# Optimization experiments

Measured on AMD Instinct MI355X. Metric: run time of the kernel, lower is better.

The kernel has to match this reference:

```python
import jax, jax.numpy as jnp
import numpy as np

V = 1024      # visible_size (channel_size)
H = 2048      # hidden_size
F = V + H     # full_size
T = 64        # timesteps
REC = 0.8     # params['lambda']


def setup_inputs() -> dict:
    key = jax.random.key(0)
    k1, k2, k3 = jax.random.split(key, 3)
    X = jax.random.normal(k1, (T, V), jnp.float32)
    # scale W so tanh does not fully saturate (fan-in scaling, like default init)
    W = jax.random.normal(k2, (F, F), jnp.float32) / np.float32(np.sqrt(F))
    b = jax.random.normal(k3, (F,), jnp.float32) * 0.01
    # Lambda: visible block = REC, hidden block = 1, diagonal of visible block = 1
    lam = jnp.concatenate(
        [jnp.full((V, V), REC, jnp.float32), jnp.ones((V, H), jnp.float32)], axis=1
    )
    lam = lam.at[jnp.arange(V), jnp.arange(V)].set(1.0)
    return {"X": X, "W": W, "b": b, "lam": lam}


def reference(X, W, b, lam):
    v = lam.shape[0]           # visible size
    one_minus_lam_vis = 1.0 - lam[:, :v]  # zero outside visible block anyway

    def step(carry, x_t):
        R, _ = carry
        WR = R @ W.T + b                      # [V, F] Linear applied row-wise
        U = lam * WR                          # gated recurrent part
        # I has x_t broadcast across rows in the visible block, zeros elsewhere
        U = U.at[:, :v].add(one_minus_lam_vis * x_t[None, :])
        R_next = jnp.tanh(U)                  # phi = torch.tanh
        return (R_next, U), None

    R0 = jnp.zeros((v, W.shape[0]), X.dtype)
    (_, U_last), _ = jax.lax.scan(step, (R0, R0), X)
    # torch.diag(U[:, :visible]) -> diagonal entries, shape [V]
    idx = jnp.arange(v)
    return U_last[idx, idx]
```

## Files before the change

### kernel.cpp

```cpp
#include <hip/hip_runtime.h>
#include <math.h>

#define V 1024
#define H 2048
#define F 3072
#define T 64
#define REC 0.8f

#define BM 128
#define BN 128
#define KT16 (F / 16)
#define NSS  (KT16 / 4)

typedef _Float16 half8 __attribute__((ext_vector_type(8)));
typedef float floatx16 __attribute__((ext_vector_type(16)));

__device__ __forceinline__ void gld16(const void* g, void* l) {
    __builtin_amdgcn_global_load_lds(
        (const __attribute__((address_space(1))) void*)g,
        (__attribute__((address_space(3))) void*)l, 16, 0, 0);
}

__device__ __forceinline__ float fast_tanh(float u) {
    float e = __expf(2.f * u);
    return 1.f - 2.f * __builtin_amdgcn_rcpf(e + 1.f);
}


__global__ __launch_bounds__(256)
void conv_w_fm(const float* __restrict__ W, _Float16* __restrict__ Wfm) {
    const int ct = blockIdx.y;
    const int ix = blockIdx.x * 256 + threadIdx.x;
    const int kt = ix >> 8;
    const int q  = ix & 255;
    const int n  = ct * 128 + ((q >> 6) & 3) * 32 + (q & 31);
    const int k0 = kt * 16 + ((q >> 5) & 1) * 8;
    const float* src = W + (size_t)n * F + k0;
    float4 v0 = *(const float4*)src;
    float4 v1 = *(const float4*)(src + 4);
    half8 o = { (_Float16)v0.x, (_Float16)v0.y, (_Float16)v0.z, (_Float16)v0.w,
                (_Float16)v1.x, (_Float16)v1.y, (_Float16)v1.z, (_Float16)v1.w };
    *(half8*)(Wfm + ((size_t)(ct * KT16 + kt) * 2048 + q * 8)) = o;
}

__global__ __launch_bounds__(256)
void init_step0(const float* __restrict__ b, const float* __restrict__ x0,
                _Float16* __restrict__ Rfm) {
    const int rt = blockIdx.y;
    const int ix = blockIdx.x * 256 + threadIdx.x;
    const int kt = ix >> 8;
    const int q  = ix & 255;
    const int gi = rt * 128 + ((q >> 6) & 3) * 32 + (q & 31);
    const int k0 = kt * 16 + ((q >> 5) & 1) * 8;
    half8 o;
    #pragma unroll
    for (int e = 0; e < 8; ++e) {
        int gj = k0 + e;
        float wr = b[gj];
        float u = (gj >= V || gi == gj) ? wr : (REC * wr + (1.f - REC) * x0[gj]);
        o[e] = (_Float16)fast_tanh(u);
    }
    *(half8*)(Rfm + ((size_t)(rt * KT16 + kt) * 2048 + q * 8)) = o;
}

__global__ __launch_bounds__(512, 2)
void frnn_step(const _Float16* __restrict__ Rin, const _Float16* __restrict__ Wfm,
               const float* __restrict__ b, const float* __restrict__ xt,
               _Float16* __restrict__ Rout, float* __restrict__ out, int is_last)
{
    __shared__ _Float16 A0[8192], B0[8192];
    __shared__ _Float16 A1[8192], B1[8192];
    __shared__ _Float16 A2[8192], B2[8192];

    const int tid  = threadIdx.x;
    const int lane = tid & 63;
    const int wid  = tid >> 6;
    const int sp   = wid & 1;
    const int kg   = wid >> 1;
    const int row0 = blockIdx.y * BM;
    const int col0 = blockIdx.x * BN;
    const int lane8 = lane * 8;

    const int sq  = tid & 255;
    const int sq8 = sq * 8;
    const _Float16* sgbase = (tid < 256)
        ? Rin + ((size_t)blockIdx.y * KT16 * 2048 + sq8)
        : Wfm + ((size_t)blockIdx.x * KT16 * 2048 + sq8);

    floatx16 acc[2][4];
    #pragma unroll
    for (int i = 0; i < 2; ++i)
        #pragma unroll
        for (int j = 0; j < 4; ++j)
            #pragma unroll
            for (int r = 0; r < 16; ++r) acc[i][j][r] = 0.f;

    half8 fa0[2], fa1[2], fb0[2], fb1[2], fb2[2], fb3[2];

    {
        _Float16* d0 = (tid < 256) ? &A0[sq8] : &B0[sq8];
        _Float16* d1 = (tid < 256) ? &A1[sq8] : &B1[sq8];
        #pragma unroll
        for (int g = 0; g < 4; ++g)
            gld16(sgbase + (size_t)g * 2048, d0 + g * 2048);
        asm volatile("" ::: "memory");
        #pragma unroll
        for (int g = 0; g < 4; ++g)
            gld16(sgbase + (size_t)(4 + g) * 2048, d1 + g * 2048);
        asm volatile("" ::: "memory");
    }
    {
        asm volatile("s_waitcnt vmcnt(4) lgkmcnt(0)\n\ts_barrier" ::: "memory");
        const _Float16* sA = &A0[kg * 2048];
        const _Float16* sB = &B0[kg * 2048];
        fa0[0] = *(const half8*)(sA + sp * 1024 + lane8);
        fa1[0] = *(const half8*)(sA + sp * 1024 + 512 + lane8);
        fb0[0] = *(const half8*)(sB + lane8);
        fb1[0] = *(const half8*)(sB + 512 + lane8);
        fb2[0] = *(const half8*)(sB + 1024 + lane8);
        fb3[0] = *(const half8*)(sB + 1536 + lane8);
        asm volatile("" ::: "memory");
        _Float16* d2 = (tid < 256) ? &A2[sq8] : &B2[sq8];
        #pragma unroll
        for (int g = 0; g < 4; ++g)
            gld16(sgbase + (size_t)(8 + g) * 2048, d2 + g * 2048);
        asm volatile("" ::: "memory");
    }

#define BODY(M, RA, RB, NA, NB, RS, CS)                                         \
  {                                                                             \
    asm volatile("s_waitcnt vmcnt(4) lgkmcnt(0)\n\ts_barrier" ::: "memory");    \
    const _Float16* sA = &RA[kg * 2048];                                        \
    const _Float16* sB = &RB[kg * 2048];                                        \
    fa0[RS] = *(const half8*)(sA + sp * 1024 + lane8);                          \
    fa1[RS] = *(const half8*)(sA + sp * 1024 + 512 + lane8);                    \
    fb0[RS] = *(const half8*)(sB + lane8);                                      \
    fb1[RS] = *(const half8*)(sB + 512 + lane8);                                \
    fb2[RS] = *(const half8*)(sB + 1024 + lane8);                               \
    fb3[RS] = *(const half8*)(sB + 1536 + lane8);                               \
    asm volatile("" ::: "memory");          \
    int nxt = (M) + 3; if (nxt >= NSS) nxt -= NSS;     \
    _Float16* dst = (tid < 256) ? &NA[sq8] : &NB[sq8];                          \
    _Pragma("unroll")                                                           \
    for (int g = 0; g < 4; ++g)                                                 \
        gld16(sgbase + (size_t)(nxt * 4 + g) * 2048, dst + g * 2048);           \
    __builtin_amdgcn_sched_barrier(0);      \
    __builtin_amdgcn_s_setprio(1);                                              \
    acc[0][0] = __builtin_amdgcn_mfma_f32_32x32x16_f16(fa0[CS], fb0[CS], acc[0][0],0,0,0);\
    acc[0][1] = __builtin_amdgcn_mfma_f32_32x32x16_f16(fa0[CS], fb1[CS], acc[0][1],0,0,0);\
    acc[0][2] = __builtin_amdgcn_mfma_f32_32x32x16_f16(fa0[CS], fb2[CS], acc[0][2],0,0,0);\
    acc[0][3] = __builtin_amdgcn_mfma_f32_32x32x16_f16(fa0[CS], fb3[CS], acc[0][3],0,0,0);\
    acc[1][0] = __builtin_amdgcn_mfma_f32_32x32x16_f16(fa1[CS], fb0[CS], acc[1][0],0,0,0);\
    acc[1][1] = __builtin_amdgcn_mfma_f32_32x32x16_f16(fa1[CS], fb1[CS], acc[1][1],0,0,0);\
    acc[1][2] = __builtin_amdgcn_mfma_f32_32x32x16_f16(fa1[CS], fb2[CS], acc[1][2],0,0,0);\
    acc[1][3] = __builtin_amdgcn_mfma_f32_32x32x16_f16(fa1[CS], fb3[CS], acc[1][3],0,0,0);\
    __builtin_amdgcn_s_setprio(0);                                              \
  }

    #pragma unroll 1
    for (int m6 = 0; m6 < NSS / 6; ++m6) {
        const int M = m6 * 6;
        BODY(M,     A1, B1, A0, B0, 1, 0)
        BODY(M + 1, A2, B2, A1, B1, 0, 1)
        BODY(M + 2, A0, B0, A2, B2, 1, 0)
        BODY(M + 3, A1, B1, A0, B0, 0, 1)
        BODY(M + 4, A2, B2, A1, B1, 1, 0)
        BODY(M + 5, A0, B0, A2, B2, 0, 1)
    }
#undef BODY

    asm volatile("s_waitcnt vmcnt(0) lgkmcnt(0)\n\ts_barrier" ::: "memory");

    const int m32 = lane & 31, hh = lane >> 5;
    float b_r[4], x_r[4];
    if (kg == 0) {
        #pragma unroll
        for (int j = 0; j < 4; ++j) {
            int gj = col0 + j * 32 + m32;
            b_r[j] = b[gj];
            x_r[j] = (gj < V) ? xt[gj] : 0.f;
        }
    }

    float* red0 = (float*)(sp ? A1 : A0);
    float* red1 = (float*)(sp ? B1 : B0);
    #pragma unroll 1
    for (int w = 1; w < 4; ++w) {
        if (kg == w) {
            #pragma unroll
            for (int j = 0; j < 4; ++j)
                #pragma unroll
                for (int q4 = 0; q4 < 4; ++q4) {
                    float4 v0 = { acc[0][j][4*q4],   acc[0][j][4*q4+1],
                                  acc[0][j][4*q4+2], acc[0][j][4*q4+3] };
                    float4 v1 = { acc[1][j][4*q4],   acc[1][j][4*q4+1],
                                  acc[1][j][4*q4+2], acc[1][j][4*q4+3] };
                    *(float4*)(red0 + (j*4 + q4) * 256 + lane * 4) = v0;
                    *(float4*)(red1 + (j*4 + q4) * 256 + lane * 4) = v1;
                }
        }
        __syncthreads();
        if (kg == 0) {
            #pragma unroll
            for (int j = 0; j < 4; ++j)
                #pragma unroll
                for (int q4 = 0; q4 < 4; ++q4) {
                    float4 v0 = *(const float4*)(red0 + (j*4 + q4) * 256 + lane * 4);
                    float4 v1 = *(const float4*)(red1 + (j*4 + q4) * 256 + lane * 4);
                    acc[0][j][4*q4]   += v0.x; acc[0][j][4*q4+1] += v0.y;
                    acc[0][j][4*q4+2] += v0.z; acc[0][j][4*q4+3] += v0.w;
                    acc[1][j][4*q4]   += v1.x; acc[1][j][4*q4+1] += v1.y;
                    acc[1][j][4*q4+2] += v1.z; acc[1][j][4*q4+3] += v1.w;
                }
        }
        __syncthreads();
    }

    if (kg == 0) {
        #pragma unroll
        for (int i = 0; i < 2; ++i) {
            const int mb = sp * 2 + i;
            #pragma unroll
            for (int j = 0; j < 4; ++j) {
                const int gj = col0 + j * 32 + m32;
                const int kt = gj >> 4;
                const int h2 = (gj >> 3) & 1;
                const int e  = gj & 7;
                _Float16* tb = Rout + ((size_t)(blockIdx.y * KT16 + kt) * 2048
                                       + (mb * 2 + h2) * 256 + e);
                const float bj = b_r[j];
                const float xj = x_r[j];
                const bool vis = (gj < V);
                #pragma unroll
                for (int r = 0; r < 16; ++r) {
                    const int mrow = 4 * hh + (r & 3) + 8 * (r >> 2);
                    const int gi = row0 + mb * 32 + mrow;
                    float wr = acc[i][j][r] + bj;
                    float u = (!vis || gi == gj) ? wr : (REC * wr + (1.f - REC) * xj);
                    tb[mrow * 8] = (_Float16)fast_tanh(u);
                    if (is_last && gi == gj) out[gi] = u;
                }
            }
        }
    }
}

extern "C" void kernel_launch(void* const* d_in, const int* in_sizes, int n_in,
                              void* d_out, int out_size, void* d_ws, size_t ws_size,
                              hipStream_t stream) {
    const float* X = (const float*)d_in[0];
    const float* W = (const float*)d_in[1];
    const float* b = (const float*)d_in[2];
    float* out = (float*)d_out;

    _Float16* Wfm = (_Float16*)d_ws;
    _Float16* Ra  = Wfm + (size_t)F * F;
    _Float16* Rb  = Ra + (size_t)V * F;

    conv_w_fm<<<dim3(192, 24), 256, 0, stream>>>(W, Wfm);
    init_step0<<<dim3(192, 8), 256, 0, stream>>>(b, X, Ra);

    for (int t = 1; t < T; ++t) {
        _Float16* Rin  = (t & 1) ? Ra : Rb;
        _Float16* Rout = (t & 1) ? Rb : Ra;
        frnn_step<<<dim3(24, 8), 512, 0, stream>>>(Rin, Wfm, b, X + (size_t)t * V,
                                                   Rout, out, t == T - 1);
    }
}
```

Measured before the change: 2.103 ms.

## Load A operand fragments directly from global into registers, bypassing LDS

The R (A) operand tiles are no longer staged through shared memory. Each wave reads its own A fragments straight from global memory into registers one stage ahead, while only the W (B) tiles keep the 3-stage global-to-LDS pipeline. This halves LDS traffic and capacity per block and relaxes the wait counts. In exchange, A loads become direct global latency on the critical path with only one stage of prefetch, and A data is duplicated across waves with no shared reuse. The reduction buffers are remapped to the remaining LDS arrays.

```diff
diff --git a/kernel.cpp b/kernel.cpp
--- a/kernel.cpp
+++ b/kernel.cpp
@@ -68,9 +68,8 @@
                const float* __restrict__ b, const float* __restrict__ xt,
                _Float16* __restrict__ Rout, float* __restrict__ out, int is_last)
 {
-    __shared__ _Float16 A0[8192], B0[8192];
-    __shared__ _Float16 A1[8192], B1[8192];
-    __shared__ _Float16 A2[8192], B2[8192];
+    __shared__ _Float16 B0[8192], B1[8192], B2[8192];
+    __shared__ _Float16 R3[8192];
 
     const int tid  = threadIdx.x;
     const int lane = tid & 63;
@@ -80,12 +79,11 @@
     const int row0 = blockIdx.y * BM;
     const int col0 = blockIdx.x * BN;
     const int lane8 = lane * 8;
-
-    const int sq  = tid & 255;
-    const int sq8 = sq * 8;
-    const _Float16* sgbase = (tid < 256)
-        ? Rin + ((size_t)blockIdx.y * KT16 * 2048 + sq8)
-        : Wfm + ((size_t)blockIdx.x * KT16 * 2048 + sq8);
+    const int t8   = tid * 8;
+
+    const _Float16* wgbase = Wfm + ((size_t)blockIdx.x * KT16 * 2048 + t8);
+    const _Float16* agbase = Rin + ((size_t)blockIdx.y * KT16 * 2048
+                                    + sp * 1024 + lane8);
 
     floatx16 acc[2][4];
     #pragma unroll
@@ -97,54 +95,49 @@
 
     half8 fa0[2], fa1[2], fb0[2], fb1[2], fb2[2], fb3[2];
 
+    gld16(wgbase,        &B0[t8]);
+    gld16(wgbase + 4096, &B0[4096 + t8]);
+    asm volatile("" ::: "memory");
     {
-        _Float16* d0 = (tid < 256) ? &A0[sq8] : &B0[sq8];
-        _Float16* d1 = (tid < 256) ? &A1[sq8] : &B1[sq8];
-        #pragma unroll
-        for (int g = 0; g < 4; ++g)
-            gld16(sgbase + (size_t)g * 2048, d0 + g * 2048);
-        asm volatile("" ::: "memory");
-        #pragma unroll
-        for (int g = 0; g < 4; ++g)
-            gld16(sgbase + (size_t)(4 + g) * 2048, d1 + g * 2048);
-        asm volatile("" ::: "memory");
-    }
+        const _Float16* ap = agbase + (size_t)kg * 2048;
+        fa0[0] = *(const half8*)ap;
+        fa1[0] = *(const half8*)(ap + 512);
+    }
+    asm volatile("" ::: "memory");
+    gld16(wgbase + 8192,        &B1[t8]);
+    gld16(wgbase + 8192 + 4096, &B1[4096 + t8]);
+    asm volatile("" ::: "memory");
+    asm volatile("s_waitcnt vmcnt(2)\n\ts_barrier" ::: "memory");
     {
-        asm volatile("s_waitcnt vmcnt(4) lgkmcnt(0)\n\ts_barrier" ::: "memory");
-        const _Float16* sA = &A0[kg * 2048];
         const _Float16* sB = &B0[kg * 2048];
-        fa0[0] = *(const half8*)(sA + sp * 1024 + lane8);
-        fa1[0] = *(const half8*)(sA + sp * 1024 + 512 + lane8);
         fb0[0] = *(const half8*)(sB + lane8);
         fb1[0] = *(const half8*)(sB + 512 + lane8);
         fb2[0] = *(const half8*)(sB + 1024 + lane8);
         fb3[0] = *(const half8*)(sB + 1536 + lane8);
-        asm volatile("" ::: "memory");
-        _Float16* d2 = (tid < 256) ? &A2[sq8] : &B2[sq8];
-        #pragma unroll
-        for (int g = 0; g < 4; ++g)
-            gld16(sgbase + (size_t)(8 + g) * 2048, d2 + g * 2048);
-        asm volatile("" ::: "memory");
-    }
-
-#define BODY(M, RA, RB, NA, NB, RS, CS)                                         \
+    }
+    asm volatile("" ::: "memory");
+    gld16(wgbase + 16384,        &B2[t8]);
+    gld16(wgbase + 16384 + 4096, &B2[4096 + t8]);
+    asm volatile("" ::: "memory");
+
+#define BODY(M, RB, NB, RS, CS)                                                 \
   {                                                                             \
-    asm volatile("s_waitcnt vmcnt(4) lgkmcnt(0)\n\ts_barrier" ::: "memory");    \
-    const _Float16* sA = &RA[kg * 2048];                                        \
+    asm volatile("s_waitcnt vmcnt(2) lgkmcnt(0)\n\ts_barrier" ::: "memory");    \
     const _Float16* sB = &RB[kg * 2048];                                        \
-    fa0[RS] = *(const half8*)(sA + sp * 1024 + lane8);                          \
-    fa1[RS] = *(const half8*)(sA + sp * 1024 + 512 + lane8);                    \
     fb0[RS] = *(const half8*)(sB + lane8);                                      \
     fb1[RS] = *(const half8*)(sB + 512 + lane8);                                \
     fb2[RS] = *(const half8*)(sB + 1024 + lane8);                               \
     fb3[RS] = *(const half8*)(sB + 1536 + lane8);                               \
-    asm volatile("" ::: "memory");          \
-    int nxt = (M) + 3; if (nxt >= NSS) nxt -= NSS;     \
-    _Float16* dst = (tid < 256) ? &NA[sq8] : &NB[sq8];                          \
-    _Pragma("unroll")                                                           \
-    for (int g = 0; g < 4; ++g)                                                 \
-        gld16(sgbase + (size_t)(nxt * 4 + g) * 2048, dst + g * 2048);           \
-    __builtin_amdgcn_sched_barrier(0);      \
+    int nxa = (M) + 1; if (nxa >= NSS) nxa -= NSS;     \
+    const _Float16* ap = agbase + (size_t)(nxa * 4 + kg) * 2048;                \
+    fa0[RS] = *(const half8*)ap;                                                \
+    fa1[RS] = *(const half8*)(ap + 512);                                        \
+    asm volatile("" ::: "memory");     \
+    int nxt = (M) + 3; if (nxt >= NSS) nxt -= NSS;                              \
+    const _Float16* wsrc = wgbase + (size_t)nxt * 8192;                         \
+    gld16(wsrc,        &NB[t8]);                                                \
+    gld16(wsrc + 4096, &NB[4096 + t8]);                                         \
+    __builtin_amdgcn_sched_barrier(0);          \
     __builtin_amdgcn_s_setprio(1);                                              \
     acc[0][0] = __builtin_amdgcn_mfma_f32_32x32x16_f16(fa0[CS], fb0[CS], acc[0][0],0,0,0);\
     acc[0][1] = __builtin_amdgcn_mfma_f32_32x32x16_f16(fa0[CS], fb1[CS], acc[0][1],0,0,0);\
@@ -160,12 +153,12 @@
     #pragma unroll 1
     for (int m6 = 0; m6 < NSS / 6; ++m6) {
         const int M = m6 * 6;
-        BODY(M,     A1, B1, A0, B0, 1, 0)
-        BODY(M + 1, A2, B2, A1, B1, 0, 1)
-        BODY(M + 2, A0, B0, A2, B2, 1, 0)
-        BODY(M + 3, A1, B1, A0, B0, 0, 1)
-        BODY(M + 4, A2, B2, A1, B1, 1, 0)
-        BODY(M + 5, A0, B0, A2, B2, 0, 1)
+        BODY(M,     B1, B0, 1, 0)
+        BODY(M + 1, B2, B1, 0, 1)
+        BODY(M + 2, B0, B2, 1, 0)
+        BODY(M + 3, B1, B0, 0, 1)
+        BODY(M + 4, B2, B1, 1, 0)
+        BODY(M + 5, B0, B2, 0, 1)
     }
 #undef BODY
 
@@ -182,8 +175,8 @@
         }
     }
 
-    float* red0 = (float*)(sp ? A1 : A0);
-    float* red1 = (float*)(sp ? B1 : B0);
+    float* red0 = (float*)(sp ? B2 : B0);
+    float* red1 = (float*)(sp ? R3 : B1);
     #pragma unroll 1
     for (int w = 1; w < 4; ++w) {
         if (kg == w) {
```

Result: slower. 2.747 ms (+30.6%).
